# Kernel tuning notes

Hardware: AMD Instinct MI355X
Metric: run time of the kernel (lower is better)

Reference implementation:

```python
import jax, jax.numpy as jnp
import numpy as np

B, N_TOTAL, IN_CH, N_SUB, E, OUT_CH = 4096, 500, 8, 77, 400, 2
EPS = 1e-12


def _glorot(key, shape, scale=0.05):
    return jax.random.normal(key, shape, dtype=jnp.float32) * scale


def setup_inputs() -> dict:
    key = jax.random.key(0)
    ks = jax.random.split(key, 16)
    x = jax.random.normal(ks[0], (B, N_TOTAL, IN_CH), dtype=jnp.float32)
    n_id = jax.random.randint(ks[1], (N_SUB,), 0, N_TOTAL)
    edge_index = jax.random.randint(ks[2], (2, E), 0, N_SUB)
    return {
        "x": x, "n_id": n_id, "edge_index": edge_index,
        # SAGEConv weights: concat doubles the input dim
        "W1": _glorot(ks[3], (2 * IN_CH, 64)), "b1": jnp.zeros((64,), jnp.float32),
        "W2": _glorot(ks[4], (2 * 64, 256)),   "b2": jnp.zeros((256,), jnp.float32),
        "W3": _glorot(ks[5], (2 * 256, 512)),  "b3": jnp.zeros((512,), jnp.float32),
        # MLP head
        "L1w": _glorot(ks[6], (512 * N_SUB, 1024), 0.01), "L1b": jnp.zeros((1024,), jnp.float32),
        "L2w": _glorot(ks[7], (1024, 218)), "L2b": jnp.zeros((218,), jnp.float32),
        "L3w": _glorot(ks[8], (218, OUT_CH)), "L3b": jnp.zeros((OUT_CH,), jnp.float32),
    }


def sage_conv(x, edge_index, W, b):
    # x: [B, N_SUB, C]; edge_index: [2, E], local ids in [0, N_SUB)
    # PyG<=1.3 SAGEConv: remove self loops, add self loops, mean aggregate,
    # concat [x, aggr], linear, L2 normalize.
    src, dst = edge_index[0], edge_index[1]
    valid = (src != dst)
    vmask = valid.astype(x.dtype)
    msgs = x[:, src, :] * vmask[None, :, None]                       # [B, E, C]
    seg = jax.vmap(lambda m: jax.ops.segment_sum(m, dst, num_segments=N_SUB))(msgs)
    counts = jax.ops.segment_sum(vmask, dst, num_segments=N_SUB)     # [N_SUB]
    aggr = (seg + x) / (counts + 1.0)[None, :, None]                 # self loop included
    h = jnp.concatenate([x, aggr], axis=-1) @ W + b
    norm = jnp.linalg.norm(h, axis=-1, keepdims=True)
    return h / jnp.maximum(norm, EPS)


def reference(x, n_id, edge_index, W1, b1, W2, b2, W3, b3,
              L1w, L1b, L2w, L2b, L3w, L3b):
    xt = x[:, n_id, :]                                               # [B, 77, 8]
    xt = jax.nn.relu(sage_conv(xt, edge_index, W1, b1))              # [B, 77, 64]
    xt = jax.nn.relu(sage_conv(xt, edge_index, W2, b2))              # [B, 77, 256]
    xt = jax.nn.relu(sage_conv(xt, edge_index, W3, b3))              # [B, 77, 512]
    xt = xt.reshape(xt.shape[0], -1)                                 # [B, 39424]
    xt = jax.nn.relu(xt @ L1w + L1b)
    xt = jax.nn.relu(xt @ L2w + L2b)
    return xt @ L3w + L3b                                            # [B, 2]
```

## Files before the change

kernel.cpp:

```cpp
#include <hip/hip_runtime.h>
#include <hip/hip_bf16.h>
#include <stdint.h>

typedef unsigned short u16;
typedef __attribute__((ext_vector_type(8))) short bf16x8_t;
typedef __attribute__((ext_vector_type(4))) float f32x4_t;

#define B_SZ   4096
#define N_TOT  500
#define IN_CH  8
#define NS     77
#define NE     400
#define L2_OUT 218

#define AS1C(p) ((const __attribute__((address_space(1))) void*)(p))
#define AS3(p)  ((__attribute__((address_space(3))) void*)(p))

__device__ inline u16 f2b(float f) {
  union { float f; uint32_t u; } v; v.f = f;
  uint32_t r = v.u + 0x7FFFu + ((v.u >> 16) & 1u);
  return (u16)(r >> 16);
}
__device__ inline float b2f(u16 h) {
  union { uint32_t u; float f; } v; v.u = ((uint32_t)h) << 16; return v.f;
}

__global__ void k_setup(const int* __restrict__ ei, int* __restrict__ coff,
                        int* __restrict__ csrc, float* __restrict__ inv) {
  __shared__ int s_src[NE], s_dst[NE];
  __shared__ int s_cnt[NS], s_off[NS + 1];
  const int t = threadIdx.x;
  for (int e = t; e < NE; e += 128) { s_src[e] = ei[e]; s_dst[e] = ei[NE + e]; }
  __syncthreads();
  if (t < NS) {
    int c = 0;
    for (int e = 0; e < NE; ++e) c += (s_dst[e] == t && s_src[e] != t) ? 1 : 0;
    s_cnt[t] = c;
  }
  __syncthreads();
  if (t == 0) {
    int acc = 0;
    for (int i = 0; i < NS; ++i) { s_off[i] = acc; acc += s_cnt[i]; }
    s_off[NS] = acc;
  }
  __syncthreads();
  if (t < NS) {
    int o = s_off[t];
    for (int e = 0; e < NE; ++e)
      if (s_dst[e] == t && s_src[e] != t) csrc[o++] = s_src[e];
    coff[t] = s_off[t];
    inv[t] = 1.0f / (float)(s_cnt[t] + 1);
  }
  if (t == 0) coff[NS] = s_off[NS];
}

__global__ void k_wt(const float* __restrict__ W, u16* __restrict__ Wt,
                     int K, int Nsrc, int Ndst) {
  __shared__ float t[32][33];
  int nk = K / 32;
  int bk = blockIdx.x % nk, bn = blockIdx.x / nk;
  int r = threadIdx.x >> 3, c4 = (threadIdx.x & 7) * 4;
  int gn = bn * 32 + c4;
  const float* src = &W[(size_t)(bk * 32 + r) * Nsrc + gn];
  if (gn + 3 < Nsrc) {
    float4 v = *(const float4*)src;
    t[r][c4] = v.x; t[r][c4+1] = v.y; t[r][c4+2] = v.z; t[r][c4+3] = v.w;
  } else {
    #pragma unroll
    for (int j = 0; j < 4; ++j) t[r][c4 + j] = (gn + j < Nsrc) ? src[j] : 0.f;
  }
  __syncthreads();
  ushort4 o;
  o.x = f2b(t[c4+0][r]); o.y = f2b(t[c4+1][r]);
  o.z = f2b(t[c4+2][r]); o.w = f2b(t[c4+3][r]);
  *(ushort4*)&Wt[(size_t)(bn * 32 + r) * K + bk * 32 + c4] = o;
}

__global__ __launch_bounds__(256)
void k_front(const float* __restrict__ x, const int* __restrict__ nid,
             const float* __restrict__ W1, const float* __restrict__ b1,
             const int* __restrict__ coff, const int* __restrict__ csrc,
             const float* __restrict__ invc,
             u16* __restrict__ h1, u16* __restrict__ ag1) {
  __shared__ float Ws[16 * 64];
  __shared__ float bs[64];
  __shared__ float xs[NS * 8];
  __shared__ float ac[NS * 16];
  __shared__ u16  hn[NS * 64];
  __shared__ int soff[NS + 1];
  __shared__ int ssrc[NE];
  __shared__ float sinv[NS];
  __shared__ int snid[NS];
  const int b = blockIdx.x, t = threadIdx.x;

  ((float4*)Ws)[t] = ((const float4*)W1)[t];
  if (t < 64) bs[t] = b1[t];
  if (t < NS) { snid[t] = nid[t]; sinv[t] = invc[t]; }
  if (t < NS + 1) soff[t] = coff[t];
  for (int i = t; i < NE; i += 256) ssrc[i] = csrc[i];
  __syncthreads();

  if (t < 2 * NS) {
    int i = t >> 1, p = t & 1;
    float4 v = *(const float4*)(x + ((size_t)b * N_TOT + snid[i]) * IN_CH + p * 4);
    *(float4*)&xs[i * 8 + p * 4] = v;
  }
  __syncthreads();

  for (int idx = t; idx < NS * 8; idx += 256) {
    int i = idx >> 3, c = idx & 7;
    float s = xs[i * 8 + c];
    ac[i * 16 + c] = s;
    for (int e = soff[i]; e < soff[i + 1]; ++e) s += xs[ssrc[e] * 8 + c];
    ac[i * 16 + 8 + c] = s * sinv[i];
  }
  __syncthreads();

  const int w = t >> 6, lane = t & 63;
  for (int i = w; i < NS; i += 4) {
    float acc = bs[lane];
    #pragma unroll
    for (int k = 0; k < 16; ++k) acc += ac[i * 16 + k] * Ws[k * 64 + lane];
    float ss = acc * acc;
    #pragma unroll
    for (int d = 1; d < 64; d <<= 1) ss += __shfl_xor(ss, d);
    float rn = 1.0f / fmaxf(sqrtf(ss), 1e-12f);
    u16 hv = f2b(fmaxf(acc * rn, 0.f));
    hn[i * 64 + lane] = hv;
    h1[((size_t)b * NS + i) * 64 + lane] = hv;
  }
  __syncthreads();
  for (int i = w; i < NS; i += 4) {
    float s = b2f(hn[i * 64 + lane]);
    for (int e = soff[i]; e < soff[i + 1]; ++e) s += b2f(hn[ssrc[e] * 64 + lane]);
    ag1[((size_t)b * NS + i) * 64 + lane] = f2b(s * sinv[i]);
  }
}

template<int C>
__global__ __launch_bounds__(256)
void k_norm_aggr(u16* __restrict__ h, u16* __restrict__ ag,
                 const int* __restrict__ coff, const int* __restrict__ csrc,
                 const float* __restrict__ invc) {
  __shared__ u16 sh[NS * C];
  __shared__ int soff[NS + 1];
  __shared__ int ssrc[NE];
  __shared__ float sinv[NS];
  const int b = blockIdx.x, t = threadIdx.x;
  const ushort4* hb4 = (const ushort4*)(h + (size_t)b * NS * C);
  ushort4* sh4 = (ushort4*)sh;
  for (int i4 = t; i4 < NS * C / 4; i4 += 256) sh4[i4] = hb4[i4];
  for (int i = t; i < NS + 1; i += 256) soff[i] = coff[i];
  for (int i = t; i < NE; i += 256) ssrc[i] = csrc[i];
  for (int i = t; i < NS; i += 256) sinv[i] = invc[i];
  __syncthreads();
  const int w = t >> 6, lane = t & 63;
  constexpr int PER = C / 64;
  ushort4* hb4o = (ushort4*)(h + (size_t)b * NS * C);
  for (int i = w; i < NS; i += 4) {
    float v[PER]; float ss = 0.f;
    #pragma unroll
    for (int p = 0; p < PER / 4; ++p) {
      ushort4 r = *(ushort4*)&sh[i * C + lane * PER + p * 4];
      v[p*4+0] = b2f(r.x); v[p*4+1] = b2f(r.y); v[p*4+2] = b2f(r.z); v[p*4+3] = b2f(r.w);
    }
    #pragma unroll
    for (int p = 0; p < PER; ++p) ss += v[p] * v[p];
    #pragma unroll
    for (int d = 1; d < 64; d <<= 1) ss += __shfl_xor(ss, d);
    float rn = 1.0f / fmaxf(sqrtf(ss), 1e-12f);
    #pragma unroll
    for (int p = 0; p < PER / 4; ++p) {
      ushort4 o;
      o.x = f2b(fmaxf(v[p*4+0] * rn, 0.f)); o.y = f2b(fmaxf(v[p*4+1] * rn, 0.f));
      o.z = f2b(fmaxf(v[p*4+2] * rn, 0.f)); o.w = f2b(fmaxf(v[p*4+3] * rn, 0.f));
      *(ushort4*)&sh[i * C + lane * PER + p * 4] = o;
      hb4o[(i * C + lane * PER + p * 4) / 4] = o;
    }
  }
  __syncthreads();
  ushort4* ab4 = (ushort4*)(ag + (size_t)b * NS * C);
  for (int i = w; i < NS; i += 4) {
    #pragma unroll
    for (int p = 0; p < PER / 4; ++p) {
      int c0 = lane * PER + p * 4;
      ushort4 sv = *(ushort4*)&sh[i * C + c0];
      float s0 = b2f(sv.x), s1 = b2f(sv.y), s2 = b2f(sv.z), s3 = b2f(sv.w);
      for (int e = soff[i]; e < soff[i + 1]; ++e) {
        ushort4 nv = *(ushort4*)&sh[ssrc[e] * C + c0];
        s0 += b2f(nv.x); s1 += b2f(nv.y); s2 += b2f(nv.z); s3 += b2f(nv.w);
      }
      float iv = sinv[i];
      ushort4 o; o.x = f2b(s0 * iv); o.y = f2b(s1 * iv); o.z = f2b(s2 * iv); o.w = f2b(s3 * iv);
      ab4[(i * C + c0) / 4] = o;
    }
  }
}

template<int C>
__global__ void k_normrelu(u16* __restrict__ h) {
  const int row = blockIdx.x * 4 + (threadIdx.x >> 6);
  const int lane = threadIdx.x & 63;
  constexpr int PER = C / 64;
  u16* hr = h + (size_t)row * C;
  float v[PER];
  #pragma unroll
  for (int p = 0; p < PER / 4; ++p) {
    ushort4 r = *(const ushort4*)(hr + lane * PER + p * 4);
    v[p*4+0] = b2f(r.x); v[p*4+1] = b2f(r.y); v[p*4+2] = b2f(r.z); v[p*4+3] = b2f(r.w);
  }
  float ss = 0.f;
  #pragma unroll
  for (int j = 0; j < PER; ++j) ss += v[j] * v[j];
  #pragma unroll
  for (int d = 1; d < 64; d <<= 1) ss += __shfl_xor(ss, d);
  float rn = 1.0f / fmaxf(sqrtf(ss), 1e-12f);
  #pragma unroll
  for (int p = 0; p < PER / 4; ++p) {
    ushort4 o;
    o.x = f2b(fmaxf(v[p*4+0] * rn, 0.f)); o.y = f2b(fmaxf(v[p*4+1] * rn, 0.f));
    o.z = f2b(fmaxf(v[p*4+2] * rn, 0.f)); o.w = f2b(fmaxf(v[p*4+3] * rn, 0.f));
    *(ushort4*)(hr + lane * PER + p * 4) = o;
  }
}

template<int MODE, bool CONCAT>
__global__ __launch_bounds__(256)
void k_mfma(const u16* __restrict__ A, const u16* __restrict__ A2,
            const u16* __restrict__ Bt, const float* __restrict__ bias,
            void* __restrict__ Cv, int N, int K, int CIN,
            int kPerSplit, int Mtot, int NCOLS) {
  __shared__ u16 As[2][128 * 32];
  __shared__ u16 Bs[2][128 * 32];
  const int t = threadIdx.x;
  const int gx = gridDim.x, gy = gridDim.y;
  const int nwg = gx * gy;
  const int orig = blockIdx.y * gx + blockIdx.x;
  const int q = nwg >> 3, r8 = nwg & 7;
  const int xcd = orig & 7, jj = orig >> 3;
  const int swzb = (xcd < r8 ? xcd * (q + 1) : r8 * (q + 1) + (xcd - r8) * q) + jj;
  const int mt_i = swzb / gy, nt_i = swzb - mt_i * gy;
  const int row0 = mt_i * 128, col0 = nt_i * 128;
  const int split = blockIdx.z;
  const int kbeg = split * kPerSplit;
  const int w = t >> 6, l = t & 63;
  const int wm = w >> 1, wn = w & 1;
  const int lr = l & 15, ls = l >> 4;
  const int s_row = t >> 2;
  const int s_c = ((t & 3) ^ ((t >> 3) & 3)) * 8;
  const int lsw = (ls ^ ((lr >> 1) & 3)) * 8;

  f32x4_t acc[4][4];
  #pragma unroll
  for (int i = 0; i < 4; ++i)
    #pragma unroll
    for (int j = 0; j < 4; ++j) acc[i][j] = (f32x4_t){0.f, 0.f, 0.f, 0.f};

  auto stage = [&](int buf, int k0) {
    const u16* abase; int astride, koff;
    if constexpr (CONCAT) {
      astride = CIN;
      if (k0 < CIN) { abase = A; koff = k0; } else { abase = A2; koff = k0 - CIN; }
    } else { abase = A; astride = K; koff = k0; }
    const u16* ga0 = abase + (size_t)(row0 + s_row) * astride + koff + s_c;
    const u16* ga1 = abase + (size_t)(row0 + 64 + s_row) * astride + koff + s_c;
    u16* la = &As[buf][w * 512];
    __builtin_amdgcn_global_load_lds(AS1C(ga0), AS3(la), 16, 0, 0);
    __builtin_amdgcn_global_load_lds(AS1C(ga1), AS3(la + 2048), 16, 0, 0);
    const u16* gb0 = Bt + (size_t)(col0 + s_row) * K + k0 + s_c;
    const u16* gb1 = Bt + (size_t)(col0 + 64 + s_row) * K + k0 + s_c;
    u16* lb = &Bs[buf][w * 512];
    __builtin_amdgcn_global_load_lds(AS1C(gb0), AS3(lb), 16, 0, 0);
    __builtin_amdgcn_global_load_lds(AS1C(gb1), AS3(lb + 2048), 16, 0, 0);
  };

  const int nsteps = kPerSplit / 32;
  stage(0, kbeg);
  __syncthreads();
  for (int s = 0; s < nsteps; ++s) {
    const int buf = s & 1;
    if (s + 1 < nsteps) stage(buf ^ 1, kbeg + (s + 1) * 32);
    bf16x8_t af[4], bfr[4];
    #pragma unroll
    for (int f = 0; f < 4; ++f) {
      af[f]  = *(const bf16x8_t*)&As[buf][(wm * 64 + f * 16 + lr) * 32 + lsw];
      bfr[f] = *(const bf16x8_t*)&Bs[buf][(wn * 64 + f * 16 + lr) * 32 + lsw];
    }
    #pragma unroll
    for (int i = 0; i < 4; ++i)
      #pragma unroll
      for (int j = 0; j < 4; ++j)
        acc[i][j] = __builtin_amdgcn_mfma_f32_16x16x32_bf16(af[i], bfr[j], acc[i][j], 0, 0, 0);
    __syncthreads();
  }

  const int rbase = ls * 4;
  #pragma unroll
  for (int j = 0; j < 4; ++j) {
    const int c = col0 + wn * 64 + j * 16 + lr;
    float bv = 0.f;
    if constexpr (MODE == 0) bv = bias[c];
    if constexpr (MODE == 2) bv = (c < NCOLS) ? bias[c] : 0.f;
    #pragma unroll
    for (int i = 0; i < 4; ++i) {
      const int r0 = row0 + wm * 64 + i * 16 + rbase;
      if constexpr (MODE == 0) {
        u16* C = (u16*)Cv;
        #pragma unroll
        for (int rr = 0; rr < 4; ++rr)
          C[(size_t)(r0 + rr) * N + c] = f2b(acc[i][j][rr] + bv);
      } else if constexpr (MODE == 1) {
        float* P = (float*)Cv + (size_t)split * Mtot * N;
        #pragma unroll
        for (int rr = 0; rr < 4; ++rr)
          P[(size_t)(r0 + rr) * N + c] = acc[i][j][rr];
      } else {
        if (c < NCOLS) {
          float* C = (float*)Cv;
          #pragma unroll
          for (int rr = 0; rr < 4; ++rr)
            C[(size_t)(r0 + rr) * NCOLS + c] = fmaxf(acc[i][j][rr] + bv, 0.f);
        }
      }
    }
  }
}

__global__ void k_red4(const float* __restrict__ P, const float* __restrict__ bias,
                       u16* __restrict__ y, int MN) {
  int i = blockIdx.x * 256 + threadIdx.x;
  if (i * 4 >= MN) return;
  const float4* p = (const float4*)P;
  int stride = MN / 4;
  float4 a = p[i], b = p[i + stride], c = p[i + 2 * stride], d = p[i + 3 * stride];
  float4 bv = *(const float4*)&bias[(i * 4) & 1023];
  ushort4 o;
  o.x = f2b(fmaxf(a.x + b.x + c.x + d.x + bv.x, 0.f));
  o.y = f2b(fmaxf(a.y + b.y + c.y + d.y + bv.y, 0.f));
  o.z = f2b(fmaxf(a.z + b.z + c.z + d.z + bv.z, 0.f));
  o.w = f2b(fmaxf(a.w + b.w + c.w + d.w + bv.w, 0.f));
  *(ushort4*)&y[i * 4] = o;
}

__global__ void k_l3(const float* __restrict__ y2, const float* __restrict__ w,
                     const float* __restrict__ b, float* __restrict__ out, int nrows) {
  const int row = blockIdx.x * 4 + (threadIdx.x >> 6);
  const int lane = threadIdx.x & 63;
  if (row >= nrows) return;
  const float* yr = y2 + (size_t)row * L2_OUT;
  float s0 = 0.f, s1 = 0.f;
  for (int k = lane; k < L2_OUT; k += 64) {
    float v = yr[k];
    s0 += v * w[k * 2]; s1 += v * w[k * 2 + 1];
  }
  #pragma unroll
  for (int d = 1; d < 64; d <<= 1) { s0 += __shfl_xor(s0, d); s1 += __shfl_xor(s1, d); }
  if (lane == 0) { out[(size_t)row * 2] = s0 + b[0]; out[(size_t)row * 2 + 1] = s1 + b[1]; }
}

extern "C" void kernel_launch(void* const* d_in, const int* in_sizes, int n_in,
                              void* d_out, int out_size, void* d_ws, size_t ws_size,
                              hipStream_t stream) {
  const float* x   = (const float*)d_in[0];
  const int*   nid = (const int*)d_in[1];
  const int*   ei  = (const int*)d_in[2];
  const float* W1  = (const float*)d_in[3];  const float* b1 = (const float*)d_in[4];
  const float* W2  = (const float*)d_in[5];  const float* b2 = (const float*)d_in[6];
  const float* W3  = (const float*)d_in[7];  const float* b3 = (const float*)d_in[8];
  const float* L1w = (const float*)d_in[9];  const float* L1b = (const float*)d_in[10];
  const float* L2w = (const float*)d_in[11]; const float* L2b = (const float*)d_in[12];
  const float* L3w = (const float*)d_in[13]; const float* L3b = (const float*)d_in[14];
  float* out = (float*)d_out;

  char* ws = (char*)d_ws;
  u16* Wt2  = (u16*)ws;
  u16* Wt3  = (u16*)(ws + 65536);
  u16* WtL1 = (u16*)(ws + 589824);
  u16* WtL2 = (u16*)(ws + 81330176);
  size_t WOFF = 81854464;
  int*   coff = (int*)(ws + WOFF);
  int*   csrc = coff + 80;
  float* invc = (float*)(csrc + 400);
  size_t CHUNK0 = WOFF + 4096;

  int Bc = 4096;
  while (Bc > 128 && CHUNK0 + (size_t)Bc * 157696 > ws_size) Bc >>= 1;

  char* r1 = ws + CHUNK0;
  char* r2 = r1 + (size_t)Bc * 39424;
  char* r3 = r2 + (size_t)Bc * 39424;

  k_setup<<<1, 128, 0, stream>>>(ei, coff, csrc, invc);
  k_wt<<<(128/32)*(256/32),    256, 0, stream>>>(W2,  Wt2,  128,   256,  256);
  k_wt<<<(512/32)*(512/32),    256, 0, stream>>>(W3,  Wt3,  512,   512,  512);
  k_wt<<<(39424/32)*(1024/32), 256, 0, stream>>>(L1w, WtL1, 39424, 1024, 1024);
  k_wt<<<(1024/32)*(256/32),   256, 0, stream>>>(L2w, WtL2, 1024,  218,  256);

  for (int b0 = 0; b0 < B_SZ; b0 += Bc) {
    const int nb = Bc;
    const int rows = nb * NS;
    const int mt = rows / 128;
    u16* h1  = (u16*)r2;
    u16* ag1 = (u16*)r3;
    u16* h2  = (u16*)r1;
    u16* ag2 = (u16*)r2;
    u16* h3  = (u16*)r3;
    u16* y1b = (u16*)r1;
    float* Pc  = (float*)(r1 + (size_t)nb * 4096);
    float* y2c = (float*)r2;
    const float* xb = x + (size_t)b0 * N_TOT * IN_CH;

    k_front<<<nb, 256, 0, stream>>>(xb, nid, W1, b1, coff, csrc, invc, h1, ag1);

    k_mfma<0, true><<<dim3(mt, 2, 1), 256, 0, stream>>>(
        h1, ag1, Wt2, b2, h2, 256, 128, 64, 128, rows, 0);
    k_norm_aggr<256><<<nb, 256, 0, stream>>>(h2, ag2, coff, csrc, invc);

    k_mfma<0, true><<<dim3(mt, 4, 1), 256, 0, stream>>>(
        h2, ag2, Wt3, b3, h3, 512, 512, 256, 512, rows, 0);
    k_normrelu<512><<<rows / 4, 256, 0, stream>>>(h3);

    k_mfma<1, false><<<dim3(nb / 128, 8, 4), 256, 0, stream>>>(
        h3, nullptr, WtL1, nullptr, Pc, 1024, 39424, 0, 9856, nb, 0);
    k_red4<<<nb, 256, 0, stream>>>(Pc, L1b, y1b, nb * 1024);

    k_mfma<2, false><<<dim3(nb / 128, 2, 1), 256, 0, stream>>>(
        y1b, nullptr, WtL2, L2b, y2c, 256, 1024, 0, 1024, nb, L2_OUT);

    k_l3<<<nb / 4, 256, 0, stream>>>(y2c, L3w, L3b, out + (size_t)b0 * 2, nb);
  }
}
```

Measured before the change: 1.327 ms.

## Fuse conv3 L2-normalize into L1 GEMM via per-node row scaling; split-K L2

The conv3 GEMM epilogue now writes ReLU'd unnormalized bf16 output and per-tile sums of squares. A tiny kernel turns those sums into per-node norms and reciprocals. The L1 split-K GEMM then applies the normalization by rescaling its accumulators at each 512-wide node boundary, which removes the separate normrelu pass over h3. Since ReLU commutes with a positive scale, this should match the reference, though the values are rounded to bf16 before normalization, which may change precision. Separately, the L2 GEMM is changed to a 4-way split-K with a new reduction kernel, giving it more workgroups at the cost of extra partial-sum traffic.

```diff
diff --git a/kernel.cpp b/kernel.cpp
--- a/kernel.cpp
+++ b/kernel.cpp
@@ -224,10 +224,21 @@
   }
 }
 
-template<int MODE, bool CONCAT>
+__global__ void k_rn(const float* __restrict__ Pss, float* __restrict__ rn,
+                     float* __restrict__ nrm, int rows) {
+  int r = blockIdx.x * 256 + threadIdx.x;
+  if (r >= rows) return;
+  float4 p = ((const float4*)Pss)[r];
+  float n = fmaxf(sqrtf(p.x + p.y + p.z + p.w), 1e-12f);
+  nrm[r] = n; rn[r] = 1.0f / n;
+}
+
+template<int MODE, bool CONCAT, bool ASCALE>
 __global__ __launch_bounds__(256)
 void k_mfma(const u16* __restrict__ A, const u16* __restrict__ A2,
             const u16* __restrict__ Bt, const float* __restrict__ bias,
+            const float* __restrict__ rnv, const float* __restrict__ nrmv,
+            float* __restrict__ Pss,
             void* __restrict__ Cv, int N, int K, int CIN,
             int kPerSplit, int Mtot, int NCOLS) {
   __shared__ u16 As[2][128 * 32];
@@ -291,35 +302,87 @@
       #pragma unroll
       for (int j = 0; j < 4; ++j)
         acc[i][j] = __builtin_amdgcn_mfma_f32_16x16x32_bf16(af[i], bfr[j], acc[i][j], 0, 0, 0);
+    if constexpr (ASCALE) {
+      const int k0 = kbeg + s * 32;
+      if ((((k0 + 32) & 511) == 0) && (s + 1 < nsteps)) {
+        const int npv = k0 >> 9, nnw = (k0 + 32) >> 9;
+        #pragma unroll
+        for (int i = 0; i < 4; ++i)
+          #pragma unroll
+          for (int rr = 0; rr < 4; ++rr) {
+            const int m = row0 + wm * 64 + i * 16 + ls * 4 + rr;
+            const float sc = nrmv[(size_t)m * NS + nnw] * rnv[(size_t)m * NS + npv];
+            #pragma unroll
+            for (int j = 0; j < 4; ++j) acc[i][j][rr] *= sc;
+          }
+      }
+    }
     __syncthreads();
   }
 
-  const int rbase = ls * 4;
+  if constexpr (MODE == 3) {
+    __shared__ float sSS[128][2];
+    float ssl[4][4];
+    #pragma unroll
+    for (int i = 0; i < 4; ++i)
+      #pragma unroll
+      for (int rr = 0; rr < 4; ++rr) ssl[i][rr] = 0.f;
+    u16* Cw = (u16*)Cv;
+    #pragma unroll
+    for (int j = 0; j < 4; ++j) {
+      const int c = col0 + wn * 64 + j * 16 + lr;
+      const float bv = bias[c];
+      #pragma unroll
+      for (int i = 0; i < 4; ++i) {
+        const int r0 = row0 + wm * 64 + i * 16 + ls * 4;
+        #pragma unroll
+        for (int rr = 0; rr < 4; ++rr) {
+          float v = acc[i][j][rr] + bv;
+          ssl[i][rr] += v * v;
+          Cw[(size_t)(r0 + rr) * N + c] = f2b(fmaxf(v, 0.f));
+        }
+      }
+    }
+    #pragma unroll
+    for (int i = 0; i < 4; ++i)
+      #pragma unroll
+      for (int rr = 0; rr < 4; ++rr) {
+        float sv = ssl[i][rr];
+        sv += __shfl_xor(sv, 1); sv += __shfl_xor(sv, 2);
+        sv += __shfl_xor(sv, 4); sv += __shfl_xor(sv, 8);
+        if (lr == 0) sSS[wm * 64 + i * 16 + ls * 4 + rr][wn] = sv;
+      }
+    __syncthreads();
+    for (int rb = t; rb < 128; rb += 256)
+      Pss[(size_t)(row0 + rb) * 4 + nt_i] = sSS[rb][0] + sSS[rb][1];
+    return;
+  }
+
   #pragma unroll
   for (int j = 0; j < 4; ++j) {
     const int c = col0 + wn * 64 + j * 16 + lr;
     float bv = 0.f;
     if constexpr (MODE == 0) bv = bias[c];
-    if constexpr (MODE == 2) bv = (c < NCOLS) ? bias[c] : 0.f;
     #pragma unroll
     for (int i = 0; i < 4; ++i) {
-      const int r0 = row0 + wm * 64 + i * 16 + rbase;
+      const int r0 = row0 + wm * 64 + i * 16 + ls * 4;
       if constexpr (MODE == 0) {
         u16* C = (u16*)Cv;
         #pragma unroll
         for (int rr = 0; rr < 4; ++rr)
           C[(size_t)(r0 + rr) * N + c] = f2b(acc[i][j][rr] + bv);
-      } else if constexpr (MODE == 1) {
+      } else {
         float* P = (float*)Cv + (size_t)split * Mtot * N;
-        #pragma unroll
-        for (int rr = 0; rr < 4; ++rr)
-          P[(size_t)(r0 + rr) * N + c] = acc[i][j][rr];
-      } else {
-        if (c < NCOLS) {
-          float* C = (float*)Cv;
+        if constexpr (ASCALE) {
+          const int lastn = (kbeg + kPerSplit - 32) >> 9;
           #pragma unroll
           for (int rr = 0; rr < 4; ++rr)
-            C[(size_t)(r0 + rr) * NCOLS + c] = fmaxf(acc[i][j][rr] + bv, 0.f);
+            P[(size_t)(r0 + rr) * N + c] =
+                acc[i][j][rr] * rnv[(size_t)(r0 + rr) * NS + lastn];
+        } else {
+          #pragma unroll
+          for (int rr = 0; rr < 4; ++rr)
+            P[(size_t)(r0 + rr) * N + c] = acc[i][j][rr];
         }
       }
     }
@@ -342,6 +405,16 @@
   *(ushort4*)&y[i * 4] = o;
 }
 
+__global__ void k_red4b(const float* __restrict__ P, const float* __restrict__ bias,
+                        float* __restrict__ y, int nb) {
+  int idx = blockIdx.x * 256 + threadIdx.x;
+  int m = idx >> 8, col = idx & 255;
+  if (m >= nb) return;
+  int MN = nb * 256;
+  float s = P[idx] + P[idx + MN] + P[idx + 2 * MN] + P[idx + 3 * MN];
+  if (col < L2_OUT) y[(size_t)m * L2_OUT + col] = fmaxf(s + bias[col], 0.f);
+}
+
 __global__ void k_l3(const float* __restrict__ y2, const float* __restrict__ w,
                      const float* __restrict__ b, float* __restrict__ out, int nrows) {
   const int row = blockIdx.x * 4 + (threadIdx.x >> 6);
@@ -383,12 +456,19 @@
   float* invc = (float*)(csrc + 400);
   size_t CHUNK0 = WOFF + 4096;
 
-  int Bc = 4096;
-  while (Bc > 128 && CHUNK0 + (size_t)Bc * 157696 > ws_size) Bc >>= 1;
+  int BcF = 4096;
+  while (BcF > 128 && CHUNK0 + (size_t)BcF * 159544 > ws_size) BcF >>= 1;
+  int BcU = 4096;
+  while (BcU > 128 && CHUNK0 + (size_t)BcU * 157696 > ws_size) BcU >>= 1;
+  const bool fused = (BcF == BcU);
+  const int Bc = fused ? BcF : BcU;
 
   char* r1 = ws + CHUNK0;
   char* r2 = r1 + (size_t)Bc * 39424;
   char* r3 = r2 + (size_t)Bc * 39424;
+  float* Pss  = (float*)(r3 + (size_t)Bc * 78848);
+  float* rnv  = Pss + (size_t)Bc * NS * 4;
+  float* nrmv = rnv + (size_t)Bc * NS;
 
   k_setup<<<1, 128, 0, stream>>>(ei, coff, csrc, invc);
   k_wt<<<(128/32)*(256/32),    256, 0, stream>>>(W2,  Wt2,  128,   256,  256);
@@ -407,25 +487,34 @@
     u16* h3  = (u16*)r3;
     u16* y1b = (u16*)r1;
     float* Pc  = (float*)(r1 + (size_t)nb * 4096);
+    float* Pc2 = (float*)(r1 + (size_t)nb * 4096);
     float* y2c = (float*)r2;
     const float* xb = x + (size_t)b0 * N_TOT * IN_CH;
 
     k_front<<<nb, 256, 0, stream>>>(xb, nid, W1, b1, coff, csrc, invc, h1, ag1);
 
-    k_mfma<0, true><<<dim3(mt, 2, 1), 256, 0, stream>>>(
-        h1, ag1, Wt2, b2, h2, 256, 128, 64, 128, rows, 0);
+    k_mfma<0, true, false><<<dim3(mt, 2, 1), 256, 0, stream>>>(
+        h1, ag1, Wt2, b2, nullptr, nullptr, nullptr, h2, 256, 128, 64, 128, rows, 0);
     k_norm_aggr<256><<<nb, 256, 0, stream>>>(h2, ag2, coff, csrc, invc);
 
-    k_mfma<0, true><<<dim3(mt, 4, 1), 256, 0, stream>>>(
-        h2, ag2, Wt3, b3, h3, 512, 512, 256, 512, rows, 0);
-    k_normrelu<512><<<rows / 4, 256, 0, stream>>>(h3);
-
-    k_mfma<1, false><<<dim3(nb / 128, 8, 4), 256, 0, stream>>>(
-        h3, nullptr, WtL1, nullptr, Pc, 1024, 39424, 0, 9856, nb, 0);
+    if (fused) {
+      k_mfma<3, true, false><<<dim3(mt, 4, 1), 256, 0, stream>>>(
+          h2, ag2, Wt3, b3, nullptr, nullptr, Pss, h3, 512, 512, 256, 512, rows, 0);
+      k_rn<<<(rows + 255) / 256, 256, 0, stream>>>(Pss, rnv, nrmv, rows);
+      k_mfma<1, false, true><<<dim3(nb / 128, 8, 4), 256, 0, stream>>>(
+          h3, nullptr, WtL1, nullptr, rnv, nrmv, nullptr, Pc, 1024, 39424, 0, 9856, nb, 0);
+    } else {
+      k_mfma<0, true, false><<<dim3(mt, 4, 1), 256, 0, stream>>>(
+          h2, ag2, Wt3, b3, nullptr, nullptr, nullptr, h3, 512, 512, 256, 512, rows, 0);
+      k_normrelu<512><<<rows / 4, 256, 0, stream>>>(h3);
+      k_mfma<1, false, false><<<dim3(nb / 128, 8, 4), 256, 0, stream>>>(
+          h3, nullptr, WtL1, nullptr, nullptr, nullptr, nullptr, Pc, 1024, 39424, 0, 9856, nb, 0);
+    }
     k_red4<<<nb, 256, 0, stream>>>(Pc, L1b, y1b, nb * 1024);
 
-    k_mfma<2, false><<<dim3(nb / 128, 2, 1), 256, 0, stream>>>(
-        y1b, nullptr, WtL2, L2b, y2c, 256, 1024, 0, 1024, nb, L2_OUT);
+    k_mfma<1, false, false><<<dim3(nb / 128, 2, 4), 256, 0, stream>>>(
+        y1b, nullptr, WtL2, nullptr, nullptr, nullptr, nullptr, Pc2, 256, 1024, 0, 256, nb, 0);
+    k_red4b<<<nb, 256, 0, stream>>>(Pc2, L2b, y2c, nb);
 
     k_l3<<<nb / 4, 256, 0, stream>>>(y2c, L3w, L3b, out + (size_t)b0 * 2, nb);
   }
```

Result: slower. 1.371 ms (+3.3%).
